# Performance work log

Hardware: AMD Instinct MI355X
Metric: run time of the kernel (lower is better)

Reference implementation:

```python
import jax, jax.numpy as jnp
import numpy as np

# ---- config (mirrors module init_kwargs) ----
PRE_NMS_TOP_N = 4096
POST_NMS_TOP_N = 300
NMS_THRESH = 0.5
MIN_SIZE = 0
IMG_H = 640
IMG_W = 640
BBOX_XFORM_CLIP = float(np.log(1000.0 / 16.0))  # exp clamp in BoxCoder.decode
NEG = -1e9  # score sentinel for suppressed boxes
TO_REMOVE = 1.0


def setup_inputs() -> dict:
    key = jax.random.key(0)
    k1, k2, k3 = jax.random.split(key, 3)
    N, A, H, W, C = 16, 3, 160, 160, 80
    objectness = jax.random.normal(k1, (N, A, H, W), jnp.float32)
    box_regression = jax.random.normal(k2, (N, A * 4, H, W), jnp.float32) * 0.5
    cls = jax.random.normal(k3, (N, A * C, H, W), jnp.float32)
    # grid anchors in xyxy, ordering matches permute_and_flatten (H, W, A)
    stride = IMG_W / W
    xs = (np.arange(W, dtype=np.float32) + 0.5) * stride
    ys = (np.arange(H, dtype=np.float32) + 0.5) * stride
    cy, cx = np.meshgrid(ys, xs, indexing="ij")  # [H,W]
    half = np.array([32.0, 64.0, 128.0], dtype=np.float32) / 2.0  # A anchor sizes
    x1 = cx[..., None] - half
    y1 = cy[..., None] - half
    x2 = cx[..., None] + half - 1.0
    y2 = cy[..., None] + half - 1.0
    anch = np.stack([x1, y1, x2, y2], axis=-1).reshape(-1, 4).astype(np.float32)
    anchors = jnp.broadcast_to(jnp.asarray(anch), (N,) + anch.shape)  # [N, A*H*W, 4]
    return {"anchors": anchors, "objectness": objectness,
            "box_regression": box_regression, "cls": cls}


def _permute_and_flatten(x, N, A, C, H, W):
    # (N, A*C, H, W) -> (N, H*W*A, C)
    return x.reshape(N, A, C, H, W).transpose(0, 3, 4, 1, 2).reshape(N, H * W * A, C)


def _decode(rel, anc):
    # BoxCoder(weights=(1,1,1,1)).decode ; rel, anc: [..., 4] xyxy anchors
    w = anc[..., 2] - anc[..., 0] + TO_REMOVE
    h = anc[..., 3] - anc[..., 1] + TO_REMOVE
    cx = anc[..., 0] + 0.5 * w
    cy = anc[..., 1] + 0.5 * h
    dx, dy = rel[..., 0], rel[..., 1]
    dw = jnp.minimum(rel[..., 2], BBOX_XFORM_CLIP)
    dh = jnp.minimum(rel[..., 3], BBOX_XFORM_CLIP)
    pcx = dx * w + cx
    pcy = dy * h + cy
    pw = jnp.exp(dw) * w
    ph = jnp.exp(dh) * h
    return jnp.stack([pcx - 0.5 * pw, pcy - 0.5 * ph,
                      pcx + 0.5 * pw - 1.0, pcy + 0.5 * ph - 1.0], axis=-1)


def _iou_one_vs_all(b, boxes):
    area_b = (b[2] - b[0] + TO_REMOVE) * (b[3] - b[1] + TO_REMOVE)
    areas = (boxes[:, 2] - boxes[:, 0] + TO_REMOVE) * (boxes[:, 3] - boxes[:, 1] + TO_REMOVE)
    iw = jnp.clip(jnp.minimum(b[2], boxes[:, 2]) - jnp.maximum(b[0], boxes[:, 0]) + TO_REMOVE, 0.0)
    ih = jnp.clip(jnp.minimum(b[3], boxes[:, 3]) - jnp.maximum(b[1], boxes[:, 1]) + TO_REMOVE, 0.0)
    inter = iw * ih
    return inter / (area_b + areas - inter)


def _nms_indices(boxes, scores):
    # greedy NMS, fixed POST_NMS_TOP_N iterations; returns (idx[K], valid[K])
    K = POST_NMS_TOP_N

    def body(i, state):
        sc, idx, val = state
        j = jnp.argmax(sc)
        s = sc[j]
        iou = _iou_one_vs_all(boxes[j], boxes)
        sc = jnp.where(iou > NMS_THRESH, NEG, sc).at[j].set(NEG)
        return sc, idx.at[i].set(j.astype(jnp.int32)), val.at[i].set(s > NEG / 2)

    idx0 = jnp.zeros((K,), jnp.int32)
    val0 = jnp.zeros((K,), bool)
    _, idx, val = jax.lax.fori_loop(0, K, body, (scores, idx0, val0))
    return idx, val


def _forward(anchors, objectness, box_regression, cls):
    N, A, H, W = objectness.shape
    C = cls.shape[1] // A
    obj = jax.nn.sigmoid(_permute_and_flatten(objectness, N, A, 1, H, W).reshape(N, -1))
    cls_f = _permute_and_flatten(cls, N, A, C, H, W)          # [N, P, C]
    reg = _permute_and_flatten(box_regression, N, A, 4, H, W)  # [N, P, 4]

    k1 = min(PRE_NMS_TOP_N, A * H * W)
    scores, topk_idx = jax.lax.top_k(obj, k1)                  # [N, K1]
    b = jnp.arange(N)[:, None]
    reg_t = reg[b, topk_idx]                                   # [N, K1, 4]
    cls_t = cls_f[b, topk_idx]                                 # [N, K1, C]
    anch_t = anchors[b, topk_idx]                              # [N, K1, 4]

    proposals = _decode(reg_t, anch_t)                         # [N, K1, 4]
    labels = jnp.argmax(cls_t, axis=-1) + 1                    # [N, K1]

    # clip_to_image(remove_empty=False)
    x1 = jnp.clip(proposals[..., 0], 0.0, IMG_W - TO_REMOVE)
    y1 = jnp.clip(proposals[..., 1], 0.0, IMG_H - TO_REMOVE)
    x2 = jnp.clip(proposals[..., 2], 0.0, IMG_W - TO_REMOVE)
    y2 = jnp.clip(proposals[..., 3], 0.0, IMG_H - TO_REMOVE)
    boxes = jnp.stack([x1, y1, x2, y2], axis=-1)

    # remove_small_boxes: keep via score masking (keeps shapes static)
    keep = ((x2 - x1 + TO_REMOVE) >= MIN_SIZE) & ((y2 - y1 + TO_REMOVE) >= MIN_SIZE)
    masked_scores = jnp.where(keep, scores, NEG)

    nms_idx, nms_valid = jax.vmap(_nms_indices)(
        jax.lax.stop_gradient(boxes), jax.lax.stop_gradient(masked_scores))

    sel_boxes = boxes[b, nms_idx]                              # [N, K2, 4]
    sel_scores = scores[b, nms_idx]                            # [N, K2]
    sel_labels = labels[b, nms_idx].astype(jnp.float32)

    sel_boxes = jnp.where(nms_valid[..., None], sel_boxes, 0.0)
    sel_scores = jnp.where(nms_valid, sel_scores, 0.0)
    sel_labels = jnp.where(nms_valid, sel_labels, 0.0)
    # [N, K2, 6] = boxes(4) | score(1) | label(1)
    return jnp.concatenate([sel_boxes, sel_scores[..., None], sel_labels[..., None]], axis=-1)


def reference(anchors, objectness, box_regression, cls):
    return _forward(anchors, objectness, box_regression, cls)
```

## Files before the change

### kernel.cpp

```cpp
#include <hip/hip_runtime.h>
#include <math.h>

#define NIMG 16
#define A_ 3
#define H_ 160
#define W_ 160
#define C_ 80
#define HW_ (H_*W_)
#define P_ (HW_*A_)
#define K1 4096
#define K2 300
#define CAND_CAP 8192
#define IMGMAX 639.0f
#define BBOX_CLIP 4.135166556742356f
#define IOU_THR (0.5 + 1.0/67108864.0)

#define RING_ROWS 128
#define GRP 16
#define NGRP (K1/GRP)
#define NTRI 2080
#define TRI_BLOCKS 520
#define NCHUNK 15

__device__ __forceinline__ unsigned int f2key(float x) {
    unsigned int u = __float_as_uint(x);
    return (u & 0x80000000u) ? ~u : (u | 0x80000000u);
}
__device__ __forceinline__ float key2f(unsigned int k) {
    unsigned int u = (k & 0x80000000u) ? (k & 0x7FFFFFFFu) : ~k;
    return __uint_as_float(u);
}

__global__ __launch_bounds__(256) void k_hist(
        const float* __restrict__ obj, unsigned int* __restrict__ hist) {
    const int n = blockIdx.x / NCHUNK;
    const int chunk = blockIdx.x % NCHUNK;
    __shared__ unsigned int lh[4096];
    const int tid = threadIdx.x;
    for (int i = tid; i < 4096; i += 256) lh[i] = 0;
    __syncthreads();
    const float4* o4 = (const float4*)(obj + (size_t)n * P_ + chunk * 5120);
    for (int q = tid; q < 1280; q += 256) {
        float4 v = o4[q];
        atomicAdd(&lh[f2key(v.x) >> 20], 1u);
        atomicAdd(&lh[f2key(v.y) >> 20], 1u);
        atomicAdd(&lh[f2key(v.z) >> 20], 1u);
        atomicAdd(&lh[f2key(v.w) >> 20], 1u);
    }
    __syncthreads();
    unsigned int* hp = hist + ((size_t)n * NCHUNK + chunk) * 4096;
    for (int i = tid; i < 4096; i += 256) hp[i] = lh[i];
}

__global__ __launch_bounds__(256) void k_thresh(
        const unsigned int* __restrict__ hist, unsigned int* __restrict__ Tarr,
        unsigned int* __restrict__ cnt) {
    const int n = blockIdx.x, tid = threadIdx.x;
    const int lane = tid & 63, wv = tid >> 6;
    __shared__ unsigned int B[4096];
    __shared__ unsigned int wtot[4];
    for (int i = tid; i < 4096; i += 256) {
        unsigned int s = 0;
        for (int ch = 0; ch < NCHUNK; ++ch)
            s += hist[((size_t)n * NCHUNK + ch) * 4096 + i];
        B[i] = s;
    }
    __syncthreads();
    unsigned int ps = 0;
    #pragma unroll
    for (int j = 0; j < 16; ++j) ps += B[16 * tid + j];
    unsigned int t2 = ps;
    for (int off = 1; off < 64; off <<= 1) {
        unsigned int u = __shfl_down(t2, off);
        if (lane + off < 64) t2 += u;
    }
    if (lane == 0) wtot[wv] = t2;
    __syncthreads();
    unsigned int higher = 0;
    for (int w = wv + 1; w < 4; ++w) higher += wtot[w];
    const unsigned int cross = higher + t2;
    const unsigned int above = cross - ps;
    if (cross >= (unsigned)K1 && above < (unsigned)K1) {
        unsigned int r = above;
        for (int j = 15; j >= 0; --j) {
            r += B[16 * tid + j];
            if (r >= (unsigned)K1) {
                Tarr[n] = ((unsigned int)(16 * tid + j)) << 20;
                break;
            }
        }
    }
    if (tid == 0) cnt[n] = 0;
}

__global__ __launch_bounds__(256) void k_compact(
        const float* __restrict__ obj, const unsigned int* __restrict__ Tarr,
        unsigned long long* __restrict__ cand, unsigned int* __restrict__ cnt) {
    const int n = blockIdx.x / 75;
    const int base = (blockIdx.x % 75) * 1024;
    const int tid = threadIdx.x, lane = tid & 63, wv = tid >> 6;
    const unsigned int T = Tarr[n];
    float4 v = ((const float4*)(obj + (size_t)n * P_ + base))[tid];
    unsigned int k0 = f2key(v.x), k1 = f2key(v.y), k2 = f2key(v.z), k3 = f2key(v.w);
    bool p0 = k0 >= T, p1 = k1 >= T, p2 = k2 >= T, p3 = k3 >= T;
    unsigned long long m0 = __ballot(p0), m1 = __ballot(p1),
                       m2 = __ballot(p2), m3 = __ballot(p3);
    __shared__ unsigned int s_wbase[4];
    __shared__ unsigned int s_cnt, s_start;
    if (tid == 0) s_cnt = 0;
    __syncthreads();
    unsigned int c0 = (unsigned)__popcll(m0), c1 = (unsigned)__popcll(m1),
                 c2 = (unsigned)__popcll(m2), c3 = (unsigned)__popcll(m3);
    if (lane == 0) s_wbase[wv] = atomicAdd(&s_cnt, c0 + c1 + c2 + c3);
    __syncthreads();
    if (tid == 0) s_start = atomicAdd(&cnt[n], s_cnt);
    __syncthreads();
    const unsigned int wb = s_start + s_wbase[wv];
    const unsigned long long below = (1ull << lane) - 1ull;
    const int q0 = base + tid * 4;
    unsigned int pos, q;
    #define EMIT(pi, ki, oi, qi)                                               \
        if (pi) {                                                              \
            pos = wb + (oi); q = (unsigned)(qi);                               \
            if (pos < CAND_CAP) {                                              \
                unsigned int p = (q % HW_) * A_ + (q / HW_);                   \
                cand[(size_t)n * CAND_CAP + pos] =                             \
                    ((unsigned long long)(~(ki)) << 32) | (unsigned long long)p;\
            }                                                                  \
        }
    EMIT(p0, k0, (unsigned)__popcll(m0 & below), q0 + 0)
    EMIT(p1, k1, c0 + (unsigned)__popcll(m1 & below), q0 + 1)
    EMIT(p2, k2, c0 + c1 + (unsigned)__popcll(m2 & below), q0 + 2)
    EMIT(p3, k3, c0 + c1 + c2 + (unsigned)__popcll(m3 & below), q0 + 3)
    #undef EMIT
}

__global__ __launch_bounds__(1024) void k_sort1(
        const unsigned long long* __restrict__ candIn,
        const unsigned int* __restrict__ cnt,
        unsigned long long* __restrict__ candOut) {
    const int n = blockIdx.x >> 1, half = blockIdx.x & 1;
    __shared__ unsigned long long S[4096];
    const int tid = threadIdx.x;
    const int wv = tid >> 6, lane = tid & 63;
    const int seg = wv * 256;
    unsigned int c = cnt[n]; if (c > CAND_CAP) c = CAND_CAP;
    const int gbase = half * 4096;
    #pragma unroll
    for (int m = 0; m < 4; ++m) {
        int t = seg + m * 64 + lane;
        int g = gbase + t;
        S[t] = (g < (int)c) ? candIn[(size_t)n * CAND_CAP + g]
                            : 0xFFFFFFFFFFFFFFFFull;
    }
    int prevCross = 1;
    for (int k = 2; k <= 4096; k <<= 1) {
        for (int j = k >> 1; j > 0; j >>= 1) {
            int cross = (j >= 256);
            if (cross || prevCross) __syncthreads();
            #pragma unroll
            for (int m = 0; m < 4; ++m) {
                int t = seg + m * 64 + lane;
                int ixj = t ^ j;
                if (ixj > t) {
                    unsigned long long a = S[t], b = S[ixj];
                    bool up = ((t & k) == 0);
                    if (half) up = !up;
                    if ((a > b) == up) { S[t] = b; S[ixj] = a; }
                }
            }
            prevCross = cross;
        }
    }
    __syncthreads();
    #pragma unroll
    for (int m = 0; m < 4; ++m) {
        int t = seg + m * 64 + lane;
        candOut[(size_t)n * CAND_CAP + gbase + t] = S[t];
    }
}

__global__ __launch_bounds__(1024) void k_sort2(
        const unsigned long long* __restrict__ cand,
        const float* __restrict__ reg,
        unsigned int* __restrict__ sidx, float* __restrict__ sscore,
        float* __restrict__ bx1, float* __restrict__ by1,
        float* __restrict__ bx2, float* __restrict__ by2,
        float* __restrict__ bar) {
#pragma clang fp contract(off)
    const int n = blockIdx.x;
    __shared__ unsigned long long S[CAND_CAP];
    const int tid = threadIdx.x;
    const int wv = tid >> 6, lane = tid & 63;
    const int seg = wv * 512;
    #pragma unroll
    for (int m = 0; m < 8; ++m) {
        int t = seg + m * 64 + lane;
        S[t] = cand[(size_t)n * CAND_CAP + t];
    }
    int prevCross = 1;
    for (int j = 4096; j > 0; j >>= 1) {
        int cross = (j >= 512);
        if (cross || prevCross) __syncthreads();
        #pragma unroll
        for (int m = 0; m < 8; ++m) {
            int t = seg + m * 64 + lane;
            int ixj = t ^ j;
            if (ixj > t) {
                unsigned long long a = S[t], b = S[ixj];
                if (a > b) { S[t] = b; S[ixj] = a; }
            }
        }
        prevCross = cross;
    }
    __syncthreads();
    #pragma unroll
    for (int i = 0; i < 4; ++i) {
        const int t = tid + 1024 * i;
        const unsigned long long s = S[t];
        const unsigned int p = (unsigned int)s;
        const size_t gid = (size_t)n * K1 + t;
        sidx[gid] = p;
        float x = key2f(~(unsigned int)(s >> 32));
        sscore[gid] = 1.0f / (1.0f + expf(-x));

        const int a  = (int)(p % 3u);
        const int hw = (int)(p / 3u);
        const int hh = hw / W_, ww = hw % W_;
        const float* rb = reg + ((size_t)n * 12 + a * 4) * HW_ + hw;
        float dx = rb[0];
        float dy = rb[HW_];
        float dw = rb[2 * HW_];
        float dh = rb[3 * HW_];

        const int half = 16 << a;
        float a0 = (float)(4 * ww + 2 - half);
        float a1 = (float)(4 * hh + 2 - half);
        float a2 = (float)(4 * ww + 2 + half - 1);
        float a3 = (float)(4 * hh + 2 + half - 1);

        float w  = a2 - a0 + 1.0f;
        float h  = a3 - a1 + 1.0f;
        float cx = a0 + 0.5f * w;
        float cy = a1 + 0.5f * h;
        float dwc = fminf(dw, BBOX_CLIP);
        float dhc = fminf(dh, BBOX_CLIP);
        float pcx = dx * w + cx;
        float pcy = dy * h + cy;
        float pw  = expf(dwc) * w;
        float ph  = expf(dhc) * h;
        float x1 = pcx - 0.5f * pw;
        float y1 = pcy - 0.5f * ph;
        float x2 = pcx + 0.5f * pw - 1.0f;
        float y2 = pcy + 0.5f * ph - 1.0f;
        x1 = fminf(fmaxf(x1, 0.0f), IMGMAX);
        y1 = fminf(fmaxf(y1, 0.0f), IMGMAX);
        x2 = fminf(fmaxf(x2, 0.0f), IMGMAX);
        y2 = fminf(fmaxf(y2, 0.0f), IMGMAX);
        bx1[gid] = x1; by1[gid] = y1; bx2[gid] = x2; by2[gid] = y2;
        bar[gid] = (x2 - x1 + 1.0f) * (y2 - y1 + 1.0f);
    }
}

__global__ __launch_bounds__(256) void k_iou(
        const float* __restrict__ bx1, const float* __restrict__ by1,
        const float* __restrict__ bx2, const float* __restrict__ by2,
        const float* __restrict__ bar,
        unsigned long long* __restrict__ mat) {
#pragma clang fp contract(off)
    const int b = blockIdx.x;
    const int n = b / TRI_BLOCKS;
    const int lane = threadIdx.x & 63, wv = threadIdx.x >> 6;
    const int t = (b % TRI_BLOCKS) * 4 + wv;
    int cw = (int)((sqrtf(8.0f * (float)t + 1.0f) - 1.0f) * 0.5f);
    while (cw * (cw + 1) / 2 > t) --cw;
    while ((cw + 1) * (cw + 2) / 2 <= t) ++cw;
    int R = t - cw * (cw + 1) / 2;
    cw = __builtin_amdgcn_readfirstlane(cw);
    R  = __builtin_amdgcn_readfirstlane(R);

    const size_t nb = (size_t)n * K1;
    const int col = cw * 64 + lane;
    const float cx1 = bx1[nb + col];
    const float cy1 = by1[nb + col];
    const float cx2 = bx2[nb + col];
    const float cy2 = by2[nb + col];
    const float ca  = bar[nb + col];

    const int rbase = R * 64;
    unsigned long long myword = 0ull;
    #pragma unroll 4
    for (int j = 0; j < 64; ++j) {
        const int r = rbase + j;
        const float rx1 = bx1[nb + r];
        const float ry1 = by1[nb + r];
        const float rx2 = bx2[nb + r];
        const float ry2 = by2[nb + r];
        const float ra  = bar[nb + r];
        float iw = fminf(rx2, cx2) - fmaxf(rx1, cx1) + 1.0f;
        float ih = fminf(ry2, cy2) - fmaxf(ry1, cy1) + 1.0f;
        iw = fmaxf(iw, 0.0f);
        ih = fmaxf(ih, 0.0f);
        float inter = iw * ih;
        float denom = (ra + ca) - inter;
        bool pred = (denom > 0.0f) && ((double)inter > (double)denom * IOU_THR);
        unsigned long long balm = __ballot(pred);
        if (lane == j) myword = balm;
    }
    mat[((size_t)n * 64 + cw) * K1 + rbase + lane] = myword;
}

__global__ __launch_bounds__(256) void k_greedy(
        const unsigned long long* __restrict__ mat, int* __restrict__ skept) {
    const int n = blockIdx.x;
    int* kp = skept + n * K2;
    const int tid = threadIdx.x, lane = tid & 63, wv = tid >> 6;
    __shared__ unsigned long long ring[RING_ROWS * 64];
    __shared__ int ctl[2];
    __shared__ int prog[3];
    volatile int* vctl = ctl;
    volatile int* vprog = prog;
    for (int k = tid; k < K2; k += 256) kp[k] = -1;
    if (tid < 3) prog[tid] = -1;
    if (tid == 0) { ctl[0] = 0; ctl[1] = 0; }
    __syncthreads();

    if (wv > 0) {
        const int pw = wv - 1;
        const unsigned long long* Mw = mat + ((size_t)n * 64 + lane) * (size_t)K1;
        for (int g = 0; g < NGRP; ++g) {
            if (((g & 7) % 3) != pw) continue;
            if (vctl[1]) return;
            int hint;
            for (;;) {
                hint = vctl[0];
                if (GRP * g <= hint + (RING_ROWS - GRP)) break;
                if (vctl[1]) return;
                __builtin_amdgcn_s_sleep(2);
            }
            if (hint >= GRP * g + GRP) {
                if (lane == 0) vprog[pw] = g;
                continue;
            }
            const int wmin = g >> 2;
            const int base = (GRP * g) & (RING_ROWS - 1);
            if (lane >= wmin) {
                const ulonglong2* p = (const ulonglong2*)(Mw + GRP * g);
                ulonglong2 tt[8];
                #pragma unroll
                for (int i = 0; i < 8; ++i) tt[i] = p[i];
                #pragma unroll
                for (int i = 0; i < 8; ++i) {
                    ring[(base + 2 * i    ) * 64 + lane] = tt[i].x;
                    ring[(base + 2 * i + 1) * 64 + lane] = tt[i].y;
                }
            }
            __asm__ __volatile__("s_waitcnt lgkmcnt(0)" ::: "memory");
            if (lane == 0) vprog[pw] = g;
        }
        return;
    }

    unsigned long long rem = 0ull;
    int cursor = 0;
    int pc0 = -1, pc1 = -1, pc2 = -1;
    for (int it = 0; it < K2; ++it) {
        const int cwrd = cursor >> 6;
        unsigned long long avail = ~rem;
        if (lane < cwrd) avail = 0ull;
        else if (lane == cwrd) avail &= ~((1ull << (cursor & 63)) - 1ull);
        unsigned long long bal = __ballot(avail != 0ull);
        if (bal == 0ull) break;
        const int L = (int)__builtin_ctzll(bal);
        unsigned long long aL = __shfl(avail, L);
        const int c = (L << 6) + (int)__builtin_ctzll(aL);
        if (lane == 0) { kp[it] = c; vctl[0] = c; }
        const int g = c >> 4;
        const int owner = (g & 7) % 3;
        unsigned long long r1 = ring[(c & (RING_ROWS - 1)) * 64 + lane];
        int pcv = (owner == 0) ? pc0 : ((owner == 1) ? pc1 : pc2);
        if (pcv < g) {
            int pv;
            while ((pv = vprog[owner]) < g) __builtin_amdgcn_s_sleep(1);
            if (owner == 0) pc0 = pv; else if (owner == 1) pc1 = pv; else pc2 = pv;
            __asm__ __volatile__("" ::: "memory");
            r1 = ring[(c & (RING_ROWS - 1)) * 64 + lane];
        }
        rem |= r1;
        cursor = c + 1;
    }
    if (lane == 0) vctl[1] = 1;
}

__global__ __launch_bounds__(256) void k_final(
        const int* __restrict__ skept, const unsigned int* __restrict__ sidx,
        const float* __restrict__ sscore, const float* __restrict__ cls,
        const float* __restrict__ bx1, const float* __restrict__ by1,
        const float* __restrict__ bx2, const float* __restrict__ by2,
        float* __restrict__ out) {
    const int g = blockIdx.x * 4 + (threadIdx.x >> 6);
    const int lane = threadIdx.x & 63;
    const int n = g / K2, k = g % K2;
    const int sel = skept[n * K2 + k];
    float* op = out + ((size_t)n * K2 + k) * 6;
    if (sel < 0) {
        if (lane < 6) op[lane] = 0.0f;
        return;
    }
    const unsigned int p = sidx[(size_t)n * K1 + sel];
    const int a  = (int)(p % 3u);
    const int hw = (int)(p / 3u);
    const float* cb = cls + ((size_t)n * 240 + a * 80) * HW_ + hw;
    float v = cb[(size_t)lane * HW_];
    int c = lane;
    if (lane < 16) {
        float v2 = cb[(size_t)(64 + lane) * HW_];
        if (v2 > v) { v = v2; c = 64 + lane; }
    }
    for (int off = 32; off > 0; off >>= 1) {
        float ov = __shfl_down(v, off);
        int   oc = __shfl_down(c, off);
        if ((ov > v) || (ov == v && oc < c)) { v = ov; c = oc; }
    }
    if (lane == 0) {
        op[0] = bx1[(size_t)n * K1 + sel];
        op[1] = by1[(size_t)n * K1 + sel];
        op[2] = bx2[(size_t)n * K1 + sel];
        op[3] = by2[(size_t)n * K1 + sel];
        op[4] = sscore[(size_t)n * K1 + sel];
        op[5] = (float)(c + 1);
    }
}

extern "C" void kernel_launch(void* const* d_in, const int* in_sizes, int n_in,
                              void* d_out, int out_size, void* d_ws, size_t ws_size,
                              hipStream_t stream) {
    (void)in_sizes; (void)n_in; (void)out_size; (void)ws_size;
    const float* objectness = (const float*)d_in[1];
    const float* box_reg    = (const float*)d_in[2];
    const float* cls        = (const float*)d_in[3];
    float* out = (float*)d_out;

    char* ws = (char*)d_ws;
    size_t off = 0;
    unsigned int* hist = (unsigned int*)(ws + off);       off += (size_t)NIMG * NCHUNK * 4096 * 4;
    unsigned int* cnt  = (unsigned int*)(ws + off);       off += 64;
    unsigned int* Tarr = (unsigned int*)(ws + off);       off += 64;
    unsigned long long* cand = (unsigned long long*)(ws + off); off += (size_t)NIMG * CAND_CAP * 8;
    unsigned int* sidx = (unsigned int*)(ws + off);       off += (size_t)NIMG * K1 * 4;
    float* sscore = (float*)(ws + off);                   off += (size_t)NIMG * K1 * 4;
    float* bx1 = (float*)(ws + off);                      off += (size_t)NIMG * K1 * 4;
    float* by1 = (float*)(ws + off);                      off += (size_t)NIMG * K1 * 4;
    float* bx2 = (float*)(ws + off);                      off += (size_t)NIMG * K1 * 4;
    float* by2 = (float*)(ws + off);                      off += (size_t)NIMG * K1 * 4;
    float* bar = (float*)(ws + off);                      off += (size_t)NIMG * K1 * 4;
    unsigned long long* mat = (unsigned long long*)(ws + off); off += (size_t)NIMG * K1 * 64 * 8;
    int* skept = (int*)(ws + off);                        off += (size_t)NIMG * K2 * 4;

    k_hist   <<<NIMG * NCHUNK, 256, 0, stream>>>(objectness, hist);
    k_thresh <<<NIMG, 256, 0, stream>>>(hist, Tarr, cnt);
    k_compact<<<NIMG * 75, 256, 0, stream>>>(objectness, Tarr, cand, cnt);
    k_sort1  <<<NIMG * 2, 1024, 0, stream>>>(cand, cnt, cand);
    k_sort2  <<<NIMG, 1024, 0, stream>>>(cand, box_reg, sidx, sscore,
                                         bx1, by1, bx2, by2, bar);
    k_iou    <<<NIMG * TRI_BLOCKS, 256, 0, stream>>>(bx1, by1, bx2, by2, bar, mat);
    k_greedy <<<NIMG, 256, 0, stream>>>(mat, skept);
    k_final  <<<NIMG * K2 / 4, 256, 0, stream>>>(skept, sidx, sscore, cls,
                                                 bx1, by1, bx2, by2, out);
}
```

Before: 761.4 us.

## Pack boxes as float4 and process two candidates per greedy NMS iteration

Replaces the four separate box coordinate arrays with one float4-packed array, so the IoU kernel and final gather each load a box with a single vector load. The greedy NMS loop now picks the next two available candidates at once and fetches both ring rows. It keeps the second candidate only if the first's row does not suppress it, which roughly halves the serial ballot/shuffle chain per kept box. The cost is more complex control flow in the serial loop and extra ring reads when the second candidate is suppressed.

```diff
diff --git a/kernel.cpp b/kernel.cpp
--- a/kernel.cpp
+++ b/kernel.cpp
@@ -184,9 +184,7 @@
         const unsigned long long* __restrict__ cand,
         const float* __restrict__ reg,
         unsigned int* __restrict__ sidx, float* __restrict__ sscore,
-        float* __restrict__ bx1, float* __restrict__ by1,
-        float* __restrict__ bx2, float* __restrict__ by2,
-        float* __restrict__ bar) {
+        float4* __restrict__ bpak, float* __restrict__ bar) {
 #pragma clang fp contract(off)
     const int n = blockIdx.x;
     __shared__ unsigned long long S[CAND_CAP];
@@ -257,15 +255,14 @@
         y1 = fminf(fmaxf(y1, 0.0f), IMGMAX);
         x2 = fminf(fmaxf(x2, 0.0f), IMGMAX);
         y2 = fminf(fmaxf(y2, 0.0f), IMGMAX);
-        bx1[gid] = x1; by1[gid] = y1; bx2[gid] = x2; by2[gid] = y2;
+        float4 b4; b4.x = x1; b4.y = y1; b4.z = x2; b4.w = y2;
+        bpak[gid] = b4;
         bar[gid] = (x2 - x1 + 1.0f) * (y2 - y1 + 1.0f);
     }
 }
 
 __global__ __launch_bounds__(256) void k_iou(
-        const float* __restrict__ bx1, const float* __restrict__ by1,
-        const float* __restrict__ bx2, const float* __restrict__ by2,
-        const float* __restrict__ bar,
+        const float4* __restrict__ bpak, const float* __restrict__ bar,
         unsigned long long* __restrict__ mat) {
 #pragma clang fp contract(off)
     const int b = blockIdx.x;
@@ -281,24 +278,19 @@
 
     const size_t nb = (size_t)n * K1;
     const int col = cw * 64 + lane;
-    const float cx1 = bx1[nb + col];
-    const float cy1 = by1[nb + col];
-    const float cx2 = bx2[nb + col];
-    const float cy2 = by2[nb + col];
+    const float4 cb = bpak[nb + col];
     const float ca  = bar[nb + col];
 
     const int rbase = R * 64;
+    const float4* rp = bpak + nb + rbase;
+    const float*  ap = bar + nb + rbase;
     unsigned long long myword = 0ull;
-    #pragma unroll 4
+    #pragma unroll 8
     for (int j = 0; j < 64; ++j) {
-        const int r = rbase + j;
-        const float rx1 = bx1[nb + r];
-        const float ry1 = by1[nb + r];
-        const float rx2 = bx2[nb + r];
-        const float ry2 = by2[nb + r];
-        const float ra  = bar[nb + r];
-        float iw = fminf(rx2, cx2) - fmaxf(rx1, cx1) + 1.0f;
-        float ih = fminf(ry2, cy2) - fmaxf(ry1, cy1) + 1.0f;
+        const float4 rb = rp[j];
+        const float  ra = ap[j];
+        float iw = fminf(rb.z, cb.z) - fmaxf(rb.x, cb.x) + 1.0f;
+        float ih = fminf(rb.w, cb.w) - fmaxf(rb.y, cb.y) + 1.0f;
         iw = fmaxf(iw, 0.0f);
         ih = fmaxf(ih, 0.0f);
         float inter = iw * ih;
@@ -363,31 +355,66 @@
 
     unsigned long long rem = 0ull;
     int cursor = 0;
-    int pc0 = -1, pc1 = -1, pc2 = -1;
-    for (int it = 0; it < K2; ++it) {
+    int pc[3] = {-1, -1, -1};
+    int it = 0;
+    while (it < K2) {
         const int cwrd = cursor >> 6;
         unsigned long long avail = ~rem;
         if (lane < cwrd) avail = 0ull;
         else if (lane == cwrd) avail &= ~((1ull << (cursor & 63)) - 1ull);
         unsigned long long bal = __ballot(avail != 0ull);
         if (bal == 0ull) break;
-        const int L = (int)__builtin_ctzll(bal);
-        unsigned long long aL = __shfl(avail, L);
-        const int c = (L << 6) + (int)__builtin_ctzll(aL);
-        if (lane == 0) { kp[it] = c; vctl[0] = c; }
-        const int g = c >> 4;
-        const int owner = (g & 7) % 3;
-        unsigned long long r1 = ring[(c & (RING_ROWS - 1)) * 64 + lane];
-        int pcv = (owner == 0) ? pc0 : ((owner == 1) ? pc1 : pc2);
-        if (pcv < g) {
+        const int L1 = (int)__builtin_ctzll(bal);
+        unsigned long long aL1 = __shfl(avail, L1);
+        const int c1 = (L1 << 6) + (int)__builtin_ctzll(aL1);
+        unsigned long long avail2 = avail;
+        if (lane == L1) avail2 &= avail2 - 1;
+        unsigned long long bal2 = __ballot(avail2 != 0ull);
+        int c2 = -1;
+        if (bal2 != 0ull && it + 1 < K2) {
+            const int L2 = (int)__builtin_ctzll(bal2);
+            unsigned long long aL2 = __shfl(avail2, L2);
+            c2 = (L2 << 6) + (int)__builtin_ctzll(aL2);
+        }
+        if (lane == 0) { kp[it] = c1; vctl[0] = c1; }
+        const int g1 = c1 >> 4, own1 = (g1 & 7) % 3;
+        unsigned long long r1 = ring[(c1 & (RING_ROWS - 1)) * 64 + lane];
+        if (pc[own1] < g1) {
             int pv;
-            while ((pv = vprog[owner]) < g) __builtin_amdgcn_s_sleep(1);
-            if (owner == 0) pc0 = pv; else if (owner == 1) pc1 = pv; else pc2 = pv;
+            while ((pv = vprog[own1]) < g1) __builtin_amdgcn_s_sleep(1);
+            pc[own1] = pv;
             __asm__ __volatile__("" ::: "memory");
-            r1 = ring[(c & (RING_ROWS - 1)) * 64 + lane];
-        }
-        rem |= r1;
-        cursor = c + 1;
+            r1 = ring[(c1 & (RING_ROWS - 1)) * 64 + lane];
+        }
+        if (c2 >= 0) {
+            __asm__ __volatile__("s_waitcnt lgkmcnt(0)" ::: "memory");
+            if (lane == 0) vctl[0] = c2;
+            const int g2 = c2 >> 4, own2 = (g2 & 7) % 3;
+            unsigned long long r2 = ring[(c2 & (RING_ROWS - 1)) * 64 + lane];
+            if (pc[own2] < g2) {
+                int pv;
+                while ((pv = vprog[own2]) < g2) __builtin_amdgcn_s_sleep(1);
+                pc[own2] = pv;
+                __asm__ __volatile__("" ::: "memory");
+                r2 = ring[(c2 & (RING_ROWS - 1)) * 64 + lane];
+            }
+            unsigned long long wsel = __shfl(r1, c2 >> 6);
+            const bool supp = (wsel >> (c2 & 63)) & 1ull;
+            rem |= r1;
+            if (!supp) {
+                rem |= r2;
+                if (lane == 0) kp[it + 1] = c2;
+                cursor = c2 + 1;
+                it += 2;
+            } else {
+                cursor = c1 + 1;
+                it += 1;
+            }
+        } else {
+            rem |= r1;
+            cursor = c1 + 1;
+            it += 1;
+        }
     }
     if (lane == 0) vctl[1] = 1;
 }
@@ -395,9 +422,7 @@
 __global__ __launch_bounds__(256) void k_final(
         const int* __restrict__ skept, const unsigned int* __restrict__ sidx,
         const float* __restrict__ sscore, const float* __restrict__ cls,
-        const float* __restrict__ bx1, const float* __restrict__ by1,
-        const float* __restrict__ bx2, const float* __restrict__ by2,
-        float* __restrict__ out) {
+        const float4* __restrict__ bpak, float* __restrict__ out) {
     const int g = blockIdx.x * 4 + (threadIdx.x >> 6);
     const int lane = threadIdx.x & 63;
     const int n = g / K2, k = g % K2;
@@ -423,10 +448,11 @@
         if ((ov > v) || (ov == v && oc < c)) { v = ov; c = oc; }
     }
     if (lane == 0) {
-        op[0] = bx1[(size_t)n * K1 + sel];
-        op[1] = by1[(size_t)n * K1 + sel];
-        op[2] = bx2[(size_t)n * K1 + sel];
-        op[3] = by2[(size_t)n * K1 + sel];
+        float4 b4 = bpak[(size_t)n * K1 + sel];
+        op[0] = b4.x;
+        op[1] = b4.y;
+        op[2] = b4.z;
+        op[3] = b4.w;
         op[4] = sscore[(size_t)n * K1 + sel];
         op[5] = (float)(c + 1);
     }
@@ -449,10 +475,7 @@
     unsigned long long* cand = (unsigned long long*)(ws + off); off += (size_t)NIMG * CAND_CAP * 8;
     unsigned int* sidx = (unsigned int*)(ws + off);       off += (size_t)NIMG * K1 * 4;
     float* sscore = (float*)(ws + off);                   off += (size_t)NIMG * K1 * 4;
-    float* bx1 = (float*)(ws + off);                      off += (size_t)NIMG * K1 * 4;
-    float* by1 = (float*)(ws + off);                      off += (size_t)NIMG * K1 * 4;
-    float* bx2 = (float*)(ws + off);                      off += (size_t)NIMG * K1 * 4;
-    float* by2 = (float*)(ws + off);                      off += (size_t)NIMG * K1 * 4;
+    float4* bpak = (float4*)(ws + off);                   off += (size_t)NIMG * K1 * 16;
     float* bar = (float*)(ws + off);                      off += (size_t)NIMG * K1 * 4;
     unsigned long long* mat = (unsigned long long*)(ws + off); off += (size_t)NIMG * K1 * 64 * 8;
     int* skept = (int*)(ws + off);                        off += (size_t)NIMG * K2 * 4;
@@ -461,10 +484,9 @@
     k_thresh <<<NIMG, 256, 0, stream>>>(hist, Tarr, cnt);
     k_compact<<<NIMG * 75, 256, 0, stream>>>(objectness, Tarr, cand, cnt);
     k_sort1  <<<NIMG * 2, 1024, 0, stream>>>(cand, cnt, cand);
-    k_sort2  <<<NIMG, 1024, 0, stream>>>(cand, box_reg, sidx, sscore,
-                                         bx1, by1, bx2, by2, bar);
-    k_iou    <<<NIMG * TRI_BLOCKS, 256, 0, stream>>>(bx1, by1, bx2, by2, bar, mat);
+    k_sort2  <<<NIMG, 1024, 0, stream>>>(cand, box_reg, sidx, sscore, bpak, bar);
+    k_iou    <<<NIMG * TRI_BLOCKS, 256, 0, stream>>>(bpak, bar, mat);
     k_greedy <<<NIMG, 256, 0, stream>>>(mat, skept);
     k_final  <<<NIMG * K2 / 4, 256, 0, stream>>>(skept, sidx, sscore, cls,
-                                                 bx1, by1, bx2, by2, out);
-}
+                                                 bpak, out);
+}
```

New measurement: 759.6 us. Within noise of the previous version (-0.2%).
